# Kernel tuning notes

Hardware: AMD Instinct MI355X
Metric: run time of the kernel (lower is better)

Reference implementation:

```python
import jax, jax.numpy as jnp
import numpy as np

N_NODES = 4096
HID = 64
N_STEP = 10
_OFFSETS = np.array([1, 2, 5, 11, 23, 47, 97, 193])  # circulant graph -> degree 16


def setup_inputs() -> dict:
    rng = np.random.default_rng(0)
    N = N_NODES
    i = np.repeat(np.arange(N), len(_OFFSETS))
    j = (i + np.tile(_OFFSETS, N)) % N
    vals = rng.normal(0.0, 0.5, i.shape).astype(np.float32)
    J = np.zeros((N, N), np.float32)
    J[i, j] = vals
    J[j, i] = vals  # symmetric coupling matrix
    row, col = np.nonzero(J)                      # E directed edges, row-major sorted
    key_fwd = row.astype(np.int64) * N + col
    rev = np.searchsorted(key_fwd, col.astype(np.int64) * N + row)  # reverse-edge index
    ru, cu = np.nonzero(np.triu(J))               # Eu upper-triangular edges
    u2e = np.searchsorted(key_fwd, ru.astype(np.int64) * N + cu)    # upper -> full edge index
    bias = rng.normal(0.0, 0.5, N).astype(np.float32)
    p = lambda *s: jnp.asarray(rng.normal(0.0, 0.1, s).astype(np.float32))
    return {
        'J': jnp.asarray(J), 'bias': jnp.asarray(bias),
        'gat_W': p(4, HID), 'gat_a': p(2 * HID, 1),
        'ci_W1': p(4, HID), 'ci_b1': jnp.zeros((HID,), jnp.float32),
        'ci_W2': p(HID, HID), 'ci_b2': jnp.zeros((HID,), jnp.float32),
        'ci_W3': p(HID, 1), 'ci_b3': jnp.zeros((1,), jnp.float32),
        'row': jnp.asarray(row.astype(np.int32)), 'col': jnp.asarray(col.astype(np.int32)),
        'rev': jnp.asarray(rev.astype(np.int32)),
        'ru': jnp.asarray(ru.astype(np.int32)), 'cu': jnp.asarray(cu.astype(np.int32)),
        'u2e': jnp.asarray(u2e.astype(np.int32)),
        'N_step': N_STEP, 'MPNNtype': 0,
    }


def reference(J, bias, gat_W, gat_a, ci_W1, ci_b1, ci_W2, ci_b2, ci_W3, ci_b3,
              row, col, rev, ru, cu, u2e, N_step, MPNNtype):
    N = J.shape[0]
    adj = (jnp.abs(J) > 0).astype(J.dtype)
    # node features: [-b, b, degree, row-sum of J]
    feat = jnp.stack([-bias, bias, adj.sum(1), J.sum(1)], axis=1)  # [N,4]
    # GAT scores: e[i,j] = leakyrelu([Wh_i || Wh_j] @ a) = leakyrelu(Wh_i@a1 + Wh_j@a2)
    Wh = feat @ gat_W                                  # [N,H]
    f1 = Wh @ gat_a[:HID, 0]
    f2 = Wh @ gat_a[HID:, 0]
    e = jax.nn.leaky_relu(f1[:, None] + f2[None, :], 0.2)
    att = jnp.where(adj > 0, jnp.exp(e), 0.0)
    Cij_matrix = 0.5 * (att + att.T)                   # [N,N]
    Cij_e = Cij_matrix[row, col]                       # [E]
    # Ci readout MLP
    h = jax.nn.relu(feat @ ci_W1 + ci_b1)
    h = jax.nn.relu(h @ ci_W2 + ci_b2)
    Ci = h @ ci_W3 + ci_b3                             # [N,1]
    dom = Ci + Cij_matrix.sum(1, keepdims=True)
    dom = jnp.sign(dom) * jnp.maximum(jnp.abs(dom), 0.1)  # clamp |.| >= 0.1
    bias_scale = bias / dom[:, 0]
    bx_scale = jnp.stack([-bias_scale, bias_scale], axis=1)  # [N,2]
    Jv = J[row, col]
    Jxy_scale = jnp.stack([jnp.stack([Jv, -Jv], -1),
                           jnp.stack([-Jv, Jv], -1)], axis=1) / Cij_e[:, None, None]  # [E,2,2]

    def node_update(em):
        # node_messages[j,:] = sum over edges (i->j) of em[e,:]
        nm = jax.ops.segment_sum(em, col, num_segments=N) / dom   # [N,2]
        lnZ = jnp.log(jnp.sum(jnp.exp(bx_scale + nm), axis=1, keepdims=True))
        return bx_scale + nm - lnZ, lnZ

    em0 = jnp.zeros((row.shape[0], 2), J.dtype)  # log of all-ones messages
    hidden0, lnZ0 = node_update(em0)

    def bp_step(carry, _):
        em, hidden, lnZ = carry
        ln_pj = hidden[row][:, :, None]     # [E,2,1]
        ln_zj = lnZ[row][:, :, None]        # [E,1,1]
        ln_mu_ij = em[rev][:, :, None]      # message on reverse edge, [E,2,1]
        M = jnp.exp(Jxy_scale + ln_pj + ln_zj - ln_mu_ij)          # [E,2,2]
        M = M / jnp.sum(jnp.max(M, axis=1), axis=1)[:, None, None]
        em_new = jnp.log(jnp.max(M ** Cij_e[:, None, None], axis=1))  # [E,2]
        hidden_new, lnZ_new = node_update(em_new)
        return (em_new, hidden_new, lnZ_new), None

    (em, hidden, lnZ), _ = jax.lax.scan(bp_step, (em0, hidden0, lnZ0), None, length=N_step)

    readout = jnp.exp(hidden)                           # [N,2]
    Js = J[ru, cu] / Cij_matrix[ru, cu]                 # [Eu]
    Jxy_u = jnp.exp(jnp.stack([jnp.stack([Js, -Js], -1),
                               jnp.stack([-Js, Js], -1)], axis=1))  # [Eu,2,2]
    temp_i = readout[cu] / jnp.exp(em[u2e])             # [Eu,2]
    temp_j = readout[ru] / jnp.exp(em[rev[u2e]])        # [Eu,2]
    pw = Jxy_u * temp_i[:, None, :] * temp_j[:, :, None]
    pw = pw / jnp.sum(pw, axis=(1, 2), keepdims=True)
    readout_pairwise = pw.reshape(-1, 4)                # [Eu,4]
    Cij_u = Cij_matrix[ru, cu]
    node_H = -jnp.sum(readout * jnp.log(readout + 1e-16), axis=1)
    edge_H = -jnp.sum(readout_pairwise * jnp.log(readout_pairwise + 1e-16), axis=1)
    node_entropy = Ci[:, 0] @ jax.lax.stop_gradient(node_H)
    edge_entropy = Cij_u @ jax.lax.stop_gradient(edge_H)
    return (readout, readout_pairwise, node_entropy + edge_entropy,
            node_entropy, edge_entropy, Ci[:, 0], Cij_u, dom)
```

## Files before the change

### kernel.cpp

```cpp
#include <hip/hip_runtime.h>
#include <cstddef>

#define TB    256
#define DEG   16
#define NSTEP 10

__global__ __launch_bounds__(TB) void k_setup(
    const float* __restrict__ J, const float* __restrict__ bias,
    const float* __restrict__ gat_W, const float* __restrict__ gat_a,
    const float* __restrict__ W1, const float* __restrict__ b1,
    const float* __restrict__ W2, const float* __restrict__ b2,
    const float* __restrict__ W3, const float* __restrict__ b3,
    const int* __restrict__ col, const int* __restrict__ rev, int N,
    int4* __restrict__ edgeP, float2* __restrict__ dbW, float2* __restrict__ uA,
    float* __restrict__ ci_out, float* __restrict__ dom_out, float* __restrict__ ent)
{
    __shared__ float sW2[64 * 64];
    __shared__ float sh1[TB / 16][65];
    const int tidb = threadIdx.x;
    const int g = blockIdx.x * TB + tidb;
    const int i = g >> 4, t = g & 15;
    const int lane = tidb & 63;

    for (int k = tidb; k < 64 * 64; k += TB) sW2[k] = W2[k];
    if (g < 3) ent[g] = 0.0f;

    const int j = col[g];
    const float Jv = J[(size_t)i * (size_t)N + (size_t)j];

    float rs = Jv;
    rs += __shfl_xor(rs, 1); rs += __shfl_xor(rs, 2);
    rs += __shfl_xor(rs, 4); rs += __shfl_xor(rs, 8);

    float rsj = 0.0f;
    {
        const int* colj = col + 16 * j;
        const float* Jrow = J + (size_t)j * (size_t)N;
        #pragma unroll 4
        for (int tt = 0; tt < 16; ++tt) rsj += Jrow[colj[tt]];
    }

    const float bi = bias[i], bj = bias[j];

    float s8 = 0.0f;
    if (lane < 8) {
        int k = lane & 3;
        const float* a = gat_a + ((lane < 4) ? 0 : 64);
        for (int h = 0; h < 64; ++h) s8 += gat_W[k * 64 + h] * a[h];
    }
    const float w10 = __shfl(s8, 0), w11 = __shfl(s8, 1), w12 = __shfl(s8, 2), w13 = __shfl(s8, 3);
    const float w20 = __shfl(s8, 4), w21 = __shfl(s8, 5), w22 = __shfl(s8, 6), w23 = __shfl(s8, 7);
    const float fd = (float)DEG;
    const float f1i = -bi * w10 + bi * w11 + fd * w12 + rs  * w13;
    const float f2i = -bi * w20 + bi * w21 + fd * w22 + rs  * w23;
    const float f1j = -bj * w10 + bj * w11 + fd * w12 + rsj * w13;
    const float f2j = -bj * w20 + bj * w21 + fd * w22 + rsj * w23;

    float x1 = f1i + f2j; x1 = (x1 > 0.0f) ? x1 : 0.2f * x1;
    float x2 = f1j + f2i; x2 = (x2 > 0.0f) ? x2 : 0.2f * x2;
    const float C  = 0.5f * (expf(x1) + expf(x2));
    const float js = Jv / C;
    edgeP[g] = make_int4(j, rev[g], __float_as_int(js), __float_as_int(C));

    float sc = C;
    sc += __shfl_xor(sc, 1); sc += __shfl_xor(sc, 2);
    sc += __shfl_xor(sc, 4); sc += __shfl_xor(sc, 8);

    const int nib = tidb >> 4;
    __syncthreads();
    #pragma unroll
    for (int m = 0; m < 4; ++m) {
        int h = t + 16 * m;
        float a = -bi * W1[h] + bi * W1[64 + h] + fd * W1[128 + h]
                + rs * W1[192 + h] + b1[h];
        sh1[nib][h] = fmaxf(a, 0.0f);
    }
    __syncthreads();
    float civ = 0.0f;
    #pragma unroll
    for (int m = 0; m < 4; ++m) {
        int o = t + 16 * m;
        float acc = b2[o];
        for (int h = 0; h < 64; ++h) acc += sh1[nib][h] * sW2[h * 64 + o];
        civ += fmaxf(acc, 0.0f) * W3[o];
    }
    civ += __shfl_xor(civ, 1); civ += __shfl_xor(civ, 2);
    civ += __shfl_xor(civ, 4); civ += __shfl_xor(civ, 8);
    const float ci = civ + b3[0];

    const float s  = ci + sc;
    const float cl = fmaxf(fabsf(s), 0.1f);
    const float d  = (s > 0.0f) ? cl : ((s < 0.0f) ? -cl : 0.0f);
    const float bs = bi / d;
    if (t == 0) {
        ci_out[i] = ci; dom_out[i] = d;
        dbW[i] = make_float2(d, bs);
        uA[i]  = make_float2(-bs, bs);
    }
}

__global__ __launch_bounds__(TB) void k_step(
    const int4* __restrict__ edgeP, const float2* __restrict__ dbW,
    const float2* __restrict__ uP, const float2* __restrict__ emP,
    float2* __restrict__ uQ, float2* __restrict__ emQ,
    int first, int last, const float* __restrict__ ci_out,
    float2* __restrict__ ro_out, float* __restrict__ ent)
{
    __shared__ float red[TB / 64];
    const int g = blockIdx.x * TB + threadIdx.x;
    const int i = g >> 4, t = g & 15;
    const int4 ep = edgeP[g];
    const int j = ep.x, rg = ep.y;
    const float js = __int_as_float(ep.z), C = __int_as_float(ep.w);

    const float2 uj = uP[j];
    float mu0 = 0.0f, mu1 = 0.0f;
    if (!first) { const float2 mu = emP[rg]; mu0 = mu.x; mu1 = mu.y; }
    const float a0 = uj.x - mu0, a1 = uj.y - mu1;
    const float t0 = fmaxf( js + a0, -js + a1);
    const float t1 = fmaxf(-js + a0,  js + a1);
    const float m2 = fmaxf(t0, t1);
    const float ls = m2 + logf(expf(t0 - m2) + expf(t1 - m2));
    const float e0 = C * (t0 - ls), e1 = C * (t1 - ls);
    emQ[g] = make_float2(e0, e1);

    float nm0 = e0, nm1 = e1;
    nm0 += __shfl_xor(nm0, 1); nm1 += __shfl_xor(nm1, 1);
    nm0 += __shfl_xor(nm0, 2); nm1 += __shfl_xor(nm1, 2);
    nm0 += __shfl_xor(nm0, 4); nm1 += __shfl_xor(nm1, 4);
    nm0 += __shfl_xor(nm0, 8); nm1 += __shfl_xor(nm1, 8);
    const float2 db = dbW[i];
    const float v0 = -db.y + nm0 / db.x, v1 = db.y + nm1 / db.x;
    if (t == 0) uQ[i] = make_float2(v0, v1);

    if (last) {
        float nodeC = 0.0f;
        if (t == 0) {
            const float mv = fmaxf(v0, v1);
            const float lz = mv + logf(expf(v0 - mv) + expf(v1 - mv));
            const float r0 = expf(v0 - lz), r1 = expf(v1 - lz);
            ro_out[i] = make_float2(r0, r1);
            const float H = -(r0 * logf(r0 + 1e-16f) + r1 * logf(r1 + 1e-16f));
            nodeC = ci_out[i] * H;
        }
        for (int off = 32; off > 0; off >>= 1) nodeC += __shfl_down(nodeC, off);
        const int lane = threadIdx.x & 63, wv = threadIdx.x >> 6;
        if (lane == 0) red[wv] = nodeC;
        __syncthreads();
        if (threadIdx.x == 0) {
            const float sn = red[0] + red[1] + red[2] + red[3];
            atomicAdd(&ent[0], sn);
            atomicAdd(&ent[1], sn);
        }
    }
}

__global__ __launch_bounds__(TB) void k_epi(
    const int* __restrict__ ru, const int* __restrict__ cu,
    const int* __restrict__ u2e, const int4* __restrict__ edgeP,
    const float2* __restrict__ uF, const float2* __restrict__ emF,
    float4* __restrict__ rp_out, float* __restrict__ cij_out,
    float* __restrict__ ent)
{
    __shared__ float red[TB / 64];
    const int u = blockIdx.x * TB + threadIdx.x;
    const int e = u2e[u], r = ru[u], c = cu[u];
    const int4 ep = edgeP[e];
    const int er = ep.y;
    const float jse = __int_as_float(ep.z), Ce = __int_as_float(ep.w);

    const float2 uc = uF[c], ur = uF[r];
    const float mc  = fmaxf(uc.x, uc.y);
    const float lc  = mc + logf(expf(uc.x - mc) + expf(uc.y - mc));
    const float mr  = fmaxf(ur.x, ur.y);
    const float lr  = mr + logf(expf(ur.x - mr) + expf(ur.y - mr));
    const float2 eme = emF[er];
    const float2 emr = emF[e];
    const float ti0 = (uc.x - lc) - eme.x, ti1 = (uc.y - lc) - eme.y;
    const float tj0 = (ur.x - lr) - emr.x, tj1 = (ur.y - lr) - emr.y;
    const float L00 =  jse + ti0 + tj0;
    const float L01 = -jse + ti1 + tj0;
    const float L10 = -jse + ti0 + tj1;
    const float L11 =  jse + ti1 + tj1;
    const float mL = fmaxf(fmaxf(L00, L01), fmaxf(L10, L11));
    float p00 = expf(L00 - mL), p01 = expf(L01 - mL);
    float p10 = expf(L10 - mL), p11 = expf(L11 - mL);
    const float inv = 1.0f / (p00 + p01 + p10 + p11);
    p00 *= inv; p01 *= inv; p10 *= inv; p11 *= inv;
    rp_out[u] = make_float4(p00, p01, p10, p11);
    cij_out[u] = Ce;
    const float H = -(p00 * logf(p00 + 1e-16f) + p01 * logf(p01 + 1e-16f)
                    + p10 * logf(p10 + 1e-16f) + p11 * logf(p11 + 1e-16f));
    float edgeC = Ce * H;
    for (int off = 32; off > 0; off >>= 1) edgeC += __shfl_down(edgeC, off);
    const int lane = threadIdx.x & 63, wv = threadIdx.x >> 6;
    if (lane == 0) red[wv] = edgeC;
    __syncthreads();
    if (threadIdx.x == 0) {
        const float se = red[0] + red[1] + red[2] + red[3];
        atomicAdd(&ent[0], se);
        atomicAdd(&ent[2], se);
    }
}

extern "C" void kernel_launch(void* const* d_in, const int* in_sizes, int n_in,
                              void* d_out, int out_size, void* d_ws, size_t ws_size,
                              hipStream_t stream) {
    const float* J     = (const float*)d_in[0];
    const float* bias  = (const float*)d_in[1];
    const float* gat_W = (const float*)d_in[2];
    const float* gat_a = (const float*)d_in[3];
    const float* W1    = (const float*)d_in[4];
    const float* b1    = (const float*)d_in[5];
    const float* W2    = (const float*)d_in[6];
    const float* b2    = (const float*)d_in[7];
    const float* W3    = (const float*)d_in[8];
    const float* b3    = (const float*)d_in[9];
    const int*   col   = (const int*)d_in[11];
    const int*   rev   = (const int*)d_in[12];
    const int*   ru    = (const int*)d_in[13];
    const int*   cu    = (const int*)d_in[14];
    const int*   u2e   = (const int*)d_in[15];

    const int N  = in_sizes[1];
    const int E  = in_sizes[10];
    const int Eu = in_sizes[13];

    float* out = (float*)d_out;
    size_t OFF_RP  = 2 * (size_t)N;
    size_t OFF_ENT = OFF_RP + 4 * (size_t)Eu;
    float2* ro_out  = (float2*)out;
    float4* rp_out  = (float4*)(out + OFF_RP);
    float*  ent     = out + OFF_ENT;
    float*  ci_out  = ent + 3;
    float*  cij_out = ci_out + N;
    float*  dom_out = cij_out + Eu;

    char* w = (char*)d_ws;
    auto carve = [&](size_t bytes) {
        void* q = (void*)w;
        w += (bytes + 255) & ~(size_t)255;
        return q;
    };
    int4*   edgeP = (int4*)carve((size_t)E * 16);
    float2* dbW   = (float2*)carve((size_t)N * 8);
    float2* uA    = (float2*)carve((size_t)N * 8);
    float2* uB    = (float2*)carve((size_t)N * 8);
    float2* emA   = (float2*)carve((size_t)E * 8);
    float2* emB   = (float2*)carve((size_t)E * 8);

    const int gE  = E / TB;
    const int gEu = Eu / TB;

    k_setup<<<gE, TB, 0, stream>>>(J, bias, gat_W, gat_a, W1, b1, W2, b2, W3, b3,
                                   col, rev, N, edgeP, dbW, uA,
                                   ci_out, dom_out, ent);

    float2 *uP = uA, *uQ = uB, *emP = emA, *emQ = emB;
    for (int s = 0; s < NSTEP; ++s) {
        const int first = (s == 0) ? 1 : 0;
        const int last  = (s == NSTEP - 1) ? 1 : 0;
        k_step<<<gE, TB, 0, stream>>>(edgeP, dbW, uP, emP, uQ, emQ,
                                      first, last, ci_out, ro_out, ent);
        float2* tp;
        tp = uP;  uP  = uQ;  uQ  = tp;
        tp = emP; emP = emQ; emQ = tp;
    }
    k_epi<<<gEu, TB, 0, stream>>>(ru, cu, u2e, edgeP, uP, emP,
                                  rp_out, cij_out, ent);
}
```

Before: 177.2 us.

## Fuse two BP steps per launch using halo recomputation in shared memory

Replaces the per-step kernel with one that runs two belief-propagation steps per launch. Each 1024-thread block recomputes the first step's messages for its 64 nodes plus a halo of neighbours in shared memory, then computes the second step locally, which halves the number of launches and global round trips. In exchange it does redundant work on the halo (480 nodes computed per 64 owned) and depends on the circulant offset structure, with a maximum offset of 193 covered by the halo, and on N being a power of two.

```diff
diff --git a/kernel.cpp b/kernel.cpp
--- a/kernel.cpp
+++ b/kernel.cpp
@@ -4,6 +4,12 @@
 #define TB    256
 #define DEG   16
 #define NSTEP 10
+
+#define TBF   1024
+#define BNODE 64
+#define HB    208
+#define HN    480
+#define HSLOT (HN * DEG)
 
 __global__ __launch_bounds__(TB) void k_setup(
     const float* __restrict__ J, const float* __restrict__ bias,
@@ -99,32 +105,72 @@
     }
 }
 
-__global__ __launch_bounds__(TB) void k_step(
-    const int4* __restrict__ edgeP, const float2* __restrict__ dbW,
-    const float2* __restrict__ uP, const float2* __restrict__ emP,
-    float2* __restrict__ uQ, float2* __restrict__ emQ,
-    int first, int last, const float* __restrict__ ci_out,
-    float2* __restrict__ ro_out, float* __restrict__ ent)
-{
-    __shared__ float red[TB / 64];
-    const int g = blockIdx.x * TB + threadIdx.x;
-    const int i = g >> 4, t = g & 15;
-    const int4 ep = edgeP[g];
-    const int j = ep.x, rg = ep.y;
-    const float js = __int_as_float(ep.z), C = __int_as_float(ep.w);
-
-    const float2 uj = uP[j];
-    float mu0 = 0.0f, mu1 = 0.0f;
-    if (!first) { const float2 mu = emP[rg]; mu0 = mu.x; mu1 = mu.y; }
+__device__ __forceinline__ float2 edge_msg(float js, float C, float2 uj,
+                                           float mu0, float mu1) {
     const float a0 = uj.x - mu0, a1 = uj.y - mu1;
     const float t0 = fmaxf( js + a0, -js + a1);
     const float t1 = fmaxf(-js + a0,  js + a1);
     const float m2 = fmaxf(t0, t1);
     const float ls = m2 + logf(expf(t0 - m2) + expf(t1 - m2));
-    const float e0 = C * (t0 - ls), e1 = C * (t1 - ls);
-    emQ[g] = make_float2(e0, e1);
-
-    float nm0 = e0, nm1 = e1;
+    return make_float2(C * (t0 - ls), C * (t1 - ls));
+}
+
+__global__ __launch_bounds__(TBF) void k_step2(
+    const int4* __restrict__ edgeP, const float2* __restrict__ dbW,
+    const float2* __restrict__ uP, const float2* __restrict__ emP,
+    float2* __restrict__ uQ, float2* __restrict__ emQ,
+    int first, int last, const float* __restrict__ ci_out,
+    float2* __restrict__ ro_out, float* __restrict__ ent, int N)
+{
+    __shared__ float2 em1[HSLOT];
+    __shared__ float2 u1[HN];
+    __shared__ float red[TBF / 64];
+    const int tidb = threadIdx.x;
+    const int mask = N - 1;
+    const int a    = blockIdx.x * BNODE;
+    const int base = (a - HB) & mask;
+
+    #pragma unroll
+    for (int k = 0; k < 8; ++k) {
+        const int slot = k * TBF + tidb;
+        float2 em; float2 uj; int jl = 0, j = 0;
+        const bool act = (slot < HSLOT);
+        if (act) {
+            jl = slot >> 4;
+            j  = (base + jl) & mask;
+            const int g = (j << 4) | (slot & 15);
+            const int4 ep = edgeP[g];
+            const float js = __int_as_float(ep.z), C = __int_as_float(ep.w);
+            uj = uP[ep.x];
+            float mu0 = 0.0f, mu1 = 0.0f;
+            if (!first) { const float2 mu = emP[ep.y]; mu0 = mu.x; mu1 = mu.y; }
+            em = edge_msg(js, C, uj, mu0, mu1);
+            em1[slot] = em;
+        } else { em = make_float2(0.0f, 0.0f); }
+        float nm0 = em.x, nm1 = em.y;
+        nm0 += __shfl_xor(nm0, 1); nm1 += __shfl_xor(nm1, 1);
+        nm0 += __shfl_xor(nm0, 2); nm1 += __shfl_xor(nm1, 2);
+        nm0 += __shfl_xor(nm0, 4); nm1 += __shfl_xor(nm1, 4);
+        nm0 += __shfl_xor(nm0, 8); nm1 += __shfl_xor(nm1, 8);
+        if (act && (slot & 15) == 0) {
+            const float2 db = dbW[j];
+            u1[jl] = make_float2(-db.y + nm0 / db.x, db.y + nm1 / db.x);
+        }
+    }
+    __syncthreads();
+
+    const int il = tidb >> 4, t = tidb & 15;
+    const int i  = a + il;
+    const int g  = (i << 4) | t;
+    const int4 ep = edgeP[g];
+    const float js = __int_as_float(ep.z), C = __int_as_float(ep.w);
+    const int jl  = (ep.x - base) & mask;
+    const float2 uj = u1[jl];
+    const float2 mu = em1[(jl << 4) | (ep.y & 15)];
+    const float2 em = edge_msg(js, C, uj, mu.x, mu.y);
+    emQ[g] = em;
+
+    float nm0 = em.x, nm1 = em.y;
     nm0 += __shfl_xor(nm0, 1); nm1 += __shfl_xor(nm1, 1);
     nm0 += __shfl_xor(nm0, 2); nm1 += __shfl_xor(nm1, 2);
     nm0 += __shfl_xor(nm0, 4); nm1 += __shfl_xor(nm1, 4);
@@ -144,11 +190,12 @@
             nodeC = ci_out[i] * H;
         }
         for (int off = 32; off > 0; off >>= 1) nodeC += __shfl_down(nodeC, off);
-        const int lane = threadIdx.x & 63, wv = threadIdx.x >> 6;
+        const int lane = tidb & 63, wv = tidb >> 6;
         if (lane == 0) red[wv] = nodeC;
         __syncthreads();
-        if (threadIdx.x == 0) {
-            const float sn = red[0] + red[1] + red[2] + red[3];
+        if (tidb == 0) {
+            float sn = 0.0f;
+            for (int w = 0; w < TBF / 64; ++w) sn += red[w];
             atomicAdd(&ent[0], sn);
             atomicAdd(&ent[1], sn);
         }
@@ -251,17 +298,18 @@
 
     const int gE  = E / TB;
     const int gEu = Eu / TB;
+    const int gF  = N / BNODE;
 
     k_setup<<<gE, TB, 0, stream>>>(J, bias, gat_W, gat_a, W1, b1, W2, b2, W3, b3,
                                    col, rev, N, edgeP, dbW, uA,
                                    ci_out, dom_out, ent);
 
     float2 *uP = uA, *uQ = uB, *emP = emA, *emQ = emB;
-    for (int s = 0; s < NSTEP; ++s) {
+    for (int s = 0; s < NSTEP / 2; ++s) {
         const int first = (s == 0) ? 1 : 0;
-        const int last  = (s == NSTEP - 1) ? 1 : 0;
-        k_step<<<gE, TB, 0, stream>>>(edgeP, dbW, uP, emP, uQ, emQ,
-                                      first, last, ci_out, ro_out, ent);
+        const int last  = (s == NSTEP / 2 - 1) ? 1 : 0;
+        k_step2<<<gF, TBF, 0, stream>>>(edgeP, dbW, uP, emP, uQ, emQ,
+                                        first, last, ci_out, ro_out, ent, N);
         float2* tp;
         tp = uP;  uP  = uQ;  uQ  = tp;
         tp = emP; emP = emQ; emQ = tp;
```

Result: slower. 200.6 us (+13.2%).
